# Kernel tuning notes

Hardware: AMD Instinct MI355X
Metric: run time of the kernel (lower is better)

The kernel has to match this reference:

```python
import jax, jax.numpy as jnp
import numpy as np

B, T, D, H = 64, 512, 256, 512  # batch, seq_len, embed_dim, enc_units


def _lstm(x_tbd, U, xW, reverse):
    """Keras LSTM with activation='sigmoid' (all gates AND candidate/output use sigmoid).
    x_tbd: [T,B,D] (only for shape), xW: precomputed x@W+b [T,B,4H], U: [H,4H].
    Gate order in Keras kernels: i, f, c(g), o."""
    if reverse:
        xW = xW[::-1]
    b = xW.shape[1]
    h0 = jnp.zeros((b, U.shape[0]), xW.dtype)
    c0 = jnp.zeros((b, U.shape[0]), xW.dtype)

    def step(carry, xw):
        h, c = carry
        z = xw + h @ U  # [B,4H]
        i, f, g, o = jnp.split(z, 4, axis=-1)
        i = jax.nn.sigmoid(i)
        f = jax.nn.sigmoid(f)
        g = jax.nn.sigmoid(g)  # activation='sigmoid' (not tanh)
        o = jax.nn.sigmoid(o)
        c_new = f * c + i * g
        h_new = o * jax.nn.sigmoid(c_new)  # activation='sigmoid' (not tanh)
        return (h_new, c_new), h_new

    (h_last, c_last), hs = jax.lax.scan(step, (h0, c0), xW)
    if reverse:
        hs = hs[::-1]  # Bidirectional re-reverses backward outputs to align in time
    return hs, h_last, c_last


def setup_inputs() -> dict:
    key = jax.random.key(0)
    ks = jax.random.split(key, 6)
    s_in = 1.0 / np.sqrt(D)
    s_rec = 1.0 / np.sqrt(H)
    return {
        "x": jax.random.normal(ks[0], (B, T, D), jnp.float32),
        "hidden": jax.random.normal(ks[1], (2 * B, H), jnp.float32),  # unused by call()
        "Wf": jax.random.normal(ks[2], (D, 4 * H), jnp.float32) * s_in,
        "Uf": jax.random.normal(ks[3], (H, 4 * H), jnp.float32) * s_rec,
        "bf": jnp.zeros((4 * H,), jnp.float32),
        "Wb": jax.random.normal(ks[4], (D, 4 * H), jnp.float32) * s_in,
        "Ub": jax.random.normal(ks[5], (H, 4 * H), jnp.float32) * s_rec,
        "bb": jnp.zeros((4 * H,), jnp.float32),
    }


def reference(x, hidden, Wf, Uf, bf, Wb, Ub, bb):
    x_tbd = jnp.transpose(x, (1, 0, 2))  # [T,B,D]
    # Precompute input projections for all timesteps (hoisted out of the scan)
    xWf = jnp.einsum('tbd,dh->tbh', x_tbd, Wf) + bf
    xWb = jnp.einsum('tbd,dh->tbh', x_tbd, Wb) + bb
    hs_f, hF, cF = _lstm(x_tbd, Uf, xWf, reverse=False)
    hs_b, hB, cB = _lstm(x_tbd, Ub, xWb, reverse=True)
    out = 0.5 * (hs_f + hs_b)  # merge_mode='ave'
    out = jnp.transpose(out, (1, 0, 2))  # [B,T,H]
    return out, hF, cF, hB, cB
```

## Files before the change

kernel.cpp:

```cpp
#include <hip/hip_runtime.h>
#include <hip/hip_bf16.h>
#include <cstdint>
#include <cstddef>

#define BB 64
#define TT 512
#define DD 256
#define HH 512
#define G4 2048

typedef __bf16 bf16x8 __attribute__((ext_vector_type(8)));
typedef __bf16 bf16x4 __attribute__((ext_vector_type(4)));
typedef float  f32x4  __attribute__((ext_vector_type(4)));
typedef unsigned long long ull_t;

#define TAGM 0xC000C000C000C000ULL

#define SPIN_CAP (1 << 16)

__device__ __forceinline__ float sigf(float x) {
  return 1.0f / (1.0f + __expf(-x));
}

__device__ __forceinline__ ull_t coh_load_u64(const __bf16* p) {
  return __hip_atomic_load(reinterpret_cast<const ull_t*>(p),
                           __ATOMIC_RELAXED, __HIP_MEMORY_SCOPE_AGENT);
}
__device__ __forceinline__ void coh_pub_u32(unsigned* p, unsigned v) {
  (void)__hip_atomic_exchange(p, v, __ATOMIC_RELAXED, __HIP_MEMORY_SCOPE_AGENT);
}

__global__ void cvt_x_kernel(const float* __restrict__ x, __bf16* __restrict__ xb) {
  int i = (blockIdx.x * 256 + threadIdx.x) * 4;
  float4 v = *(const float4*)(x + i);
  bf16x4 o;
  o[0] = (__bf16)v.x; o[1] = (__bf16)v.y; o[2] = (__bf16)v.z; o[3] = (__bf16)v.w;
  *(bf16x4*)(xb + i) = o;
}

__launch_bounds__(256, 1)
__global__ void lstm_kernel(const __bf16* __restrict__ xb,
                            const float* __restrict__ Wf, const float* __restrict__ Uf,
                            const float* __restrict__ bf_,
                            const float* __restrict__ Wb, const float* __restrict__ Ub,
                            const float* __restrict__ bb_,
                            __bf16* __restrict__ hbuf,
                            float* __restrict__ out,
                            __bf16* __restrict__ hsb) {
  const int bx  = blockIdx.x;
  const int dir = bx >> 5;
  const int s   = bx & 31;
  const float* Wd = dir ? Wb : Wf;
  const float* Ud = dir ? Ub : Uf;
  const float* bd = dir ? bb_ : bf_;
  __bf16* hb = hbuf + (size_t)dir * 2 * BB * HH;

  const int tid  = threadIdx.x;
  const int mt   = tid >> 6;
  const int lane = tid & 63;
  const int j    = lane & 15;
  const int q    = lane >> 4;
  const int colg = s * 16 + j;

  bf16x8 wfrag[4][24];
#pragma unroll
  for (int g = 0; g < 4; ++g) {
    const int col = g * HH + colg;
#pragma unroll
    for (int kt = 0; kt < 24; ++kt) {
      bf16x8 v;
#pragma unroll
      for (int e = 0; e < 8; ++e) {
        const int k = kt * 32 + q * 8 + e;
        const float w = (k < DD) ? Wd[(size_t)k * G4 + col]
                                 : Ud[(size_t)(k - DD) * G4 + col];
        v[e] = (__bf16)w;
      }
      wfrag[g][kt] = v;
    }
  }
  float bg[4];
#pragma unroll
  for (int g = 0; g < 4; ++g) bg[g] = bd[g * HH + colg];

  float cst[4] = {0.f, 0.f, 0.f, 0.f};
  const size_t outTail = (size_t)BB * TT * HH;

  for (int tau = 0; tau < TT; ++tau) {
    const int t = dir ? (TT - 1 - tau) : tau;

    const __bf16* xrow = xb + ((size_t)(mt * 16 + j) * TT + t) * DD + q * 8;
    f32x4 acc[4];
#pragma unroll
    for (int g = 0; g < 4; ++g) acc[g] = (f32x4){bg[g], bg[g], bg[g], bg[g]};
#pragma unroll
    for (int kt = 0; kt < 8; ++kt) {
      bf16x8 a = *(const bf16x8*)(xrow + kt * 32);
#pragma unroll
      for (int g = 0; g < 4; ++g)
        acc[g] = __builtin_amdgcn_mfma_f32_16x16x32_bf16(a, wfrag[g][kt], acc[g], 0, 0, 0);
    }

    if (tau) {
      const __bf16* hrow = hb + (size_t)(tau & 1) * (BB * HH)
                              + (size_t)(mt * 16 + j) * HH + q * 8;
      const ull_t epat = (ull_t)(1u + ((unsigned)(tau >> 1) & 1u)) * 0x4000400040004000ULL;
      ull_t cur[8], nxt[8];
#pragma unroll
      for (int i = 0; i < 4; ++i) {
        cur[2*i]   = coh_load_u64(hrow + i * 32);
        cur[2*i+1] = coh_load_u64(hrow + i * 32 + 4);
      }
#pragma unroll
      for (int kb = 0; kb < 4; ++kb) {
        if (kb < 3) {
#pragma unroll
          for (int i = 0; i < 4; ++i) {
            nxt[2*i]   = coh_load_u64(hrow + ((kb + 1) * 4 + i) * 32);
            nxt[2*i+1] = coh_load_u64(hrow + ((kb + 1) * 4 + i) * 32 + 4);
          }
        }
        int guard = 0;
        for (;;) {
          int ok = 1;
#pragma unroll
          for (int i = 0; i < 8; ++i) ok &= ((cur[i] & TAGM) == epat);
          if (__all(ok)) break;
          if (++guard > SPIN_CAP) break;
          __builtin_amdgcn_s_sleep(2);
#pragma unroll
          for (int i = 0; i < 4; ++i) {
            cur[2*i]   = coh_load_u64(hrow + (kb * 4 + i) * 32);
            cur[2*i+1] = coh_load_u64(hrow + (kb * 4 + i) * 32 + 4);
          }
        }
#pragma unroll
        for (int i = 0; i < 4; ++i) {
          union { ull_t u[2]; bf16x8 v; } uu;
          uu.u[0] = cur[2*i]   & ~TAGM;
          uu.u[1] = cur[2*i+1] & ~TAGM;
          const int kt = kb * 4 + i;
#pragma unroll
          for (int g = 0; g < 4; ++g)
            acc[g] = __builtin_amdgcn_mfma_f32_16x16x32_bf16(uu.v, wfrag[g][8 + kt], acc[g], 0, 0, 0);
        }
        if (kb < 3) {
#pragma unroll
          for (int i = 0; i < 8; ++i) cur[i] = nxt[i];
        }
      }
    }

    const unsigned ptag =
        ((1u + ((unsigned)((tau + 1) >> 1) & 1u)) << 14);
    __bf16* hnext = hb + (size_t)((tau + 1) & 1) * (BB * HH);
    unsigned myv[4];
#pragma unroll
    for (int r = 0; r < 4; ++r) {
      const float zi = acc[0][r], zf = acc[1][r], zg = acc[2][r], zo = acc[3][r];
      const float gi = sigf(zi), gf = sigf(zf), gg = sigf(zg), go = sigf(zo);
      const float cn = gf * cst[r] + gi * gg;
      cst[r] = cn;
      const float hn = go * sigf(cn);
      union { __bf16 b; unsigned short u; } cv;
      cv.b = (__bf16)hn;
      myv[r] = (unsigned)cv.u | ptag;
      const int orow = mt * 16 + q * 4 + r;
      if (dir == 0) {
        out[(size_t)orow * (TT * HH) + (size_t)t * HH + colg] = 0.5f * hn;
      } else {
        hsb[(size_t)t * (BB * HH) + (size_t)orow * HH + colg] = (__bf16)hn;
      }
      if (tau == TT - 1) {
        float* base = out + outTail + (size_t)dir * (2 * BB * HH);
        base[(size_t)orow * HH + colg] = hn;
        base[(size_t)BB * HH + (size_t)orow * HH + colg] = cn;
      }
    }

    unsigned pr[4];
#pragma unroll
    for (int r = 0; r < 4; ++r) pr[r] = __shfl_xor((int)myv[r], 1);
    if ((lane & 1) == 0) {
#pragma unroll
      for (int r = 0; r < 4; ++r) {
        const int orow = mt * 16 + q * 4 + r;
        unsigned pk = (myv[r] & 0xFFFFu) | (pr[r] << 16);
        coh_pub_u32((unsigned*)&hnext[(size_t)orow * HH + colg], pk);
      }
    }
  }
}

__global__ void combine_kernel(float* __restrict__ out, const __bf16* __restrict__ hsb) {
  const size_t i = ((size_t)blockIdx.x * 256 + threadIdx.x) * 4;
  const size_t b = i >> 18;
  const size_t t = (i >> 9) & 511;
  const size_t c = i & 511;
  bf16x4 hv = *(const bf16x4*)(hsb + t * (BB * HH) + b * HH + c);
  float4 v = *(float4*)(out + i);
  v.x += 0.5f * (float)hv[0];
  v.y += 0.5f * (float)hv[1];
  v.z += 0.5f * (float)hv[2];
  v.w += 0.5f * (float)hv[3];
  *(float4*)(out + i) = v;
}

extern "C" void kernel_launch(void* const* d_in, const int* in_sizes, int n_in,
                              void* d_out, int out_size, void* d_ws, size_t ws_size,
                              hipStream_t stream) {
  (void)in_sizes; (void)n_in; (void)out_size; (void)ws_size;
  const float* x   = (const float*)d_in[0];
  const float* Wf  = (const float*)d_in[2];
  const float* Uf  = (const float*)d_in[3];
  const float* bf_ = (const float*)d_in[4];
  const float* Wb  = (const float*)d_in[5];
  const float* Ub  = (const float*)d_in[6];
  const float* bb_ = (const float*)d_in[7];
  float* out = (float*)d_out;
  char* ws = (char*)d_ws;

  __bf16* hbuf = (__bf16*)(ws + 1024);
  __bf16* xb   = (__bf16*)(ws + (1 << 19));
  __bf16* hsb  = (__bf16*)(ws + (1 << 19) + (size_t)BB * TT * DD * 2);

  hipMemsetAsync(ws, 0xFF, 1 << 19, stream);
  cvt_x_kernel<<<dim3((BB * TT * DD) / 1024), dim3(256), 0, stream>>>(x, xb);
  lstm_kernel<<<dim3(64), dim3(256), 0, stream>>>(xb, Wf, Uf, bf_, Wb, Ub, bb_,
                                                  hbuf, out, hsb);
  combine_kernel<<<dim3((BB * TT * HH) / 1024), dim3(256), 0, stream>>>(out, hsb);
}
```

Before: 3.971 ms.

## Split LSTM recurrent K-reduction across two wave groups with LDS partial sums

Doubles the block to 512 threads and splits the K dimension of each timestep's gate matmul between two halves. One half computes the input projection plus the first 128 hidden columns, the other computes the remaining 384 hidden columns. Partial accumulators are reduced through shared memory after a __syncthreads. The goal is to halve the per-wave MFMA chain and register footprint on the serial critical path. The cost is an extra block-wide barrier and LDS traffic every step, with an uneven work split between the halves.

```diff
diff --git a/kernel.cpp b/kernel.cpp
--- a/kernel.cpp
+++ b/kernel.cpp
@@ -38,7 +38,7 @@
   *(bf16x4*)(xb + i) = o;
 }
 
-__launch_bounds__(256, 1)
+__launch_bounds__(512, 1)
 __global__ void lstm_kernel(const __bf16* __restrict__ xb,
                             const float* __restrict__ Wf, const float* __restrict__ Uf,
                             const float* __restrict__ bf_,
@@ -56,22 +56,26 @@
   __bf16* hb = hbuf + (size_t)dir * 2 * BB * HH;
 
   const int tid  = threadIdx.x;
-  const int mt   = tid >> 6;
+  const int mt   = (tid >> 6) & 3;
+  const int half = tid >> 8;
   const int lane = tid & 63;
   const int j    = lane & 15;
   const int q    = lane >> 4;
   const int colg = s * 16 + j;
 
-  bf16x8 wfrag[4][24];
+  __shared__ f32x4 partial[2][4][4][64];
+
+  bf16x8 wfrag[4][12];
 #pragma unroll
   for (int g = 0; g < 4; ++g) {
     const int col = g * HH + colg;
 #pragma unroll
-    for (int kt = 0; kt < 24; ++kt) {
+    for (int kt = 0; kt < 12; ++kt) {
+      const int ktg = half * 12 + kt;
       bf16x8 v;
 #pragma unroll
       for (int e = 0; e < 8; ++e) {
-        const int k = kt * 32 + q * 8 + e;
+        const int k = ktg * 32 + q * 8 + e;
         const float w = (k < DD) ? Wd[(size_t)k * G4 + col]
                                  : Ud[(size_t)(k - DD) * G4 + col];
         v[e] = (__bf16)w;
@@ -88,37 +92,28 @@
 
   for (int tau = 0; tau < TT; ++tau) {
     const int t = dir ? (TT - 1 - tau) : tau;
-
-    const __bf16* xrow = xb + ((size_t)(mt * 16 + j) * TT + t) * DD + q * 8;
+    const __bf16* hrow = hb + (size_t)(tau & 1) * (BB * HH)
+                            + (size_t)(mt * 16 + j) * HH + q * 8;
+    const ull_t epat = (ull_t)(1u + ((unsigned)(tau >> 1) & 1u)) * 0x4000400040004000ULL;
+
     f32x4 acc[4];
-#pragma unroll
-    for (int g = 0; g < 4; ++g) acc[g] = (f32x4){bg[g], bg[g], bg[g], bg[g]};
-#pragma unroll
-    for (int kt = 0; kt < 8; ++kt) {
-      bf16x8 a = *(const bf16x8*)(xrow + kt * 32);
-#pragma unroll
-      for (int g = 0; g < 4; ++g)
-        acc[g] = __builtin_amdgcn_mfma_f32_16x16x32_bf16(a, wfrag[g][kt], acc[g], 0, 0, 0);
-    }
-
-    if (tau) {
-      const __bf16* hrow = hb + (size_t)(tau & 1) * (BB * HH)
-                              + (size_t)(mt * 16 + j) * HH + q * 8;
-      const ull_t epat = (ull_t)(1u + ((unsigned)(tau >> 1) & 1u)) * 0x4000400040004000ULL;
-      ull_t cur[8], nxt[8];
-#pragma unroll
-      for (int i = 0; i < 4; ++i) {
-        cur[2*i]   = coh_load_u64(hrow + i * 32);
-        cur[2*i+1] = coh_load_u64(hrow + i * 32 + 4);
-      }
-#pragma unroll
-      for (int kb = 0; kb < 4; ++kb) {
-        if (kb < 3) {
-#pragma unroll
-          for (int i = 0; i < 4; ++i) {
-            nxt[2*i]   = coh_load_u64(hrow + ((kb + 1) * 4 + i) * 32);
-            nxt[2*i+1] = coh_load_u64(hrow + ((kb + 1) * 4 + i) * 32 + 4);
-          }
+    if (half == 0) {
+      const __bf16* xrow = xb + ((size_t)(mt * 16 + j) * TT + t) * DD + q * 8;
+#pragma unroll
+      for (int g = 0; g < 4; ++g) acc[g] = (f32x4){bg[g], bg[g], bg[g], bg[g]};
+#pragma unroll
+      for (int kt = 0; kt < 8; ++kt) {
+        bf16x8 a = *(const bf16x8*)(xrow + kt * 32);
+#pragma unroll
+        for (int g = 0; g < 4; ++g)
+          acc[g] = __builtin_amdgcn_mfma_f32_16x16x32_bf16(a, wfrag[g][kt], acc[g], 0, 0, 0);
+      }
+      if (tau) {
+        ull_t cur[8];
+#pragma unroll
+        for (int i = 0; i < 4; ++i) {
+          cur[2*i]   = coh_load_u64(hrow + i * 32);
+          cur[2*i+1] = coh_load_u64(hrow + i * 32 + 4);
         }
         int guard = 0;
         for (;;) {
@@ -130,8 +125,8 @@
           __builtin_amdgcn_s_sleep(2);
 #pragma unroll
           for (int i = 0; i < 4; ++i) {
-            cur[2*i]   = coh_load_u64(hrow + (kb * 4 + i) * 32);
-            cur[2*i+1] = coh_load_u64(hrow + (kb * 4 + i) * 32 + 4);
+            cur[2*i]   = coh_load_u64(hrow + i * 32);
+            cur[2*i+1] = coh_load_u64(hrow + i * 32 + 4);
           }
         }
 #pragma unroll
@@ -139,54 +134,107 @@
           union { ull_t u[2]; bf16x8 v; } uu;
           uu.u[0] = cur[2*i]   & ~TAGM;
           uu.u[1] = cur[2*i+1] & ~TAGM;
-          const int kt = kb * 4 + i;
 #pragma unroll
           for (int g = 0; g < 4; ++g)
-            acc[g] = __builtin_amdgcn_mfma_f32_16x16x32_bf16(uu.v, wfrag[g][8 + kt], acc[g], 0, 0, 0);
-        }
-        if (kb < 3) {
-#pragma unroll
-          for (int i = 0; i < 8; ++i) cur[i] = nxt[i];
-        }
-      }
+            acc[g] = __builtin_amdgcn_mfma_f32_16x16x32_bf16(uu.v, wfrag[g][8 + i], acc[g], 0, 0, 0);
+        }
+      }
+    } else {
+#pragma unroll
+      for (int g = 0; g < 4; ++g) acc[g] = (f32x4){0.f, 0.f, 0.f, 0.f};
+      if (tau) {
+        const __bf16* hrow1 = hrow + 128;
+        ull_t cur[8], nxt[8];
+#pragma unroll
+        for (int i = 0; i < 4; ++i) {
+          cur[2*i]   = coh_load_u64(hrow1 + i * 32);
+          cur[2*i+1] = coh_load_u64(hrow1 + i * 32 + 4);
+        }
+#pragma unroll
+        for (int kb = 0; kb < 3; ++kb) {
+          if (kb < 2) {
+#pragma unroll
+            for (int i = 0; i < 4; ++i) {
+              nxt[2*i]   = coh_load_u64(hrow1 + ((kb + 1) * 4 + i) * 32);
+              nxt[2*i+1] = coh_load_u64(hrow1 + ((kb + 1) * 4 + i) * 32 + 4);
+            }
+          }
+          int guard = 0;
+          for (;;) {
+            int ok = 1;
+#pragma unroll
+            for (int i = 0; i < 8; ++i) ok &= ((cur[i] & TAGM) == epat);
+            if (__all(ok)) break;
+            if (++guard > SPIN_CAP) break;
+            __builtin_amdgcn_s_sleep(2);
+#pragma unroll
+            for (int i = 0; i < 4; ++i) {
+              cur[2*i]   = coh_load_u64(hrow1 + (kb * 4 + i) * 32);
+              cur[2*i+1] = coh_load_u64(hrow1 + (kb * 4 + i) * 32 + 4);
+            }
+          }
+#pragma unroll
+          for (int i = 0; i < 4; ++i) {
+            union { ull_t u[2]; bf16x8 v; } uu;
+            uu.u[0] = cur[2*i]   & ~TAGM;
+            uu.u[1] = cur[2*i+1] & ~TAGM;
+#pragma unroll
+            for (int g = 0; g < 4; ++g)
+              acc[g] = __builtin_amdgcn_mfma_f32_16x16x32_bf16(uu.v, wfrag[g][kb * 4 + i], acc[g], 0, 0, 0);
+          }
+          if (kb < 2) {
+#pragma unroll
+            for (int i = 0; i < 8; ++i) cur[i] = nxt[i];
+          }
+        }
+      }
+#pragma unroll
+      for (int g = 0; g < 4; ++g) partial[tau & 1][mt][g][lane] = acc[g];
     }
 
-    const unsigned ptag =
-        ((1u + ((unsigned)((tau + 1) >> 1) & 1u)) << 14);
-    __bf16* hnext = hb + (size_t)((tau + 1) & 1) * (BB * HH);
-    unsigned myv[4];
-#pragma unroll
-    for (int r = 0; r < 4; ++r) {
-      const float zi = acc[0][r], zf = acc[1][r], zg = acc[2][r], zo = acc[3][r];
-      const float gi = sigf(zi), gf = sigf(zf), gg = sigf(zg), go = sigf(zo);
-      const float cn = gf * cst[r] + gi * gg;
-      cst[r] = cn;
-      const float hn = go * sigf(cn);
-      union { __bf16 b; unsigned short u; } cv;
-      cv.b = (__bf16)hn;
-      myv[r] = (unsigned)cv.u | ptag;
-      const int orow = mt * 16 + q * 4 + r;
-      if (dir == 0) {
-        out[(size_t)orow * (TT * HH) + (size_t)t * HH + colg] = 0.5f * hn;
-      } else {
-        hsb[(size_t)t * (BB * HH) + (size_t)orow * HH + colg] = (__bf16)hn;
-      }
-      if (tau == TT - 1) {
-        float* base = out + outTail + (size_t)dir * (2 * BB * HH);
-        base[(size_t)orow * HH + colg] = hn;
-        base[(size_t)BB * HH + (size_t)orow * HH + colg] = cn;
-      }
-    }
-
-    unsigned pr[4];
-#pragma unroll
-    for (int r = 0; r < 4; ++r) pr[r] = __shfl_xor((int)myv[r], 1);
-    if ((lane & 1) == 0) {
+    __syncthreads();
+
+    if (half == 0) {
+#pragma unroll
+      for (int g = 0; g < 4; ++g) {
+        f32x4 p = partial[tau & 1][mt][g][lane];
+        acc[g] += p;
+      }
+      const unsigned ptag = ((1u + ((unsigned)((tau + 1) >> 1) & 1u)) << 14);
+      __bf16* hnext = hb + (size_t)((tau + 1) & 1) * (BB * HH);
+      unsigned myv[4];
 #pragma unroll
       for (int r = 0; r < 4; ++r) {
+        const float zi = acc[0][r], zf = acc[1][r], zg = acc[2][r], zo = acc[3][r];
+        const float gi = sigf(zi), gf = sigf(zf), gg = sigf(zg), go = sigf(zo);
+        const float cn = gf * cst[r] + gi * gg;
+        cst[r] = cn;
+        const float hn = go * sigf(cn);
+        union { __bf16 b; unsigned short u; } cv;
+        cv.b = (__bf16)hn;
+        myv[r] = (unsigned)cv.u | ptag;
         const int orow = mt * 16 + q * 4 + r;
-        unsigned pk = (myv[r] & 0xFFFFu) | (pr[r] << 16);
-        coh_pub_u32((unsigned*)&hnext[(size_t)orow * HH + colg], pk);
+        if (dir == 0) {
+          out[(size_t)orow * (TT * HH) + (size_t)t * HH + colg] = 0.5f * hn;
+        } else {
+          hsb[(size_t)t * (BB * HH) + (size_t)orow * HH + colg] = (__bf16)hn;
+        }
+        if (tau == TT - 1) {
+          float* base = out + outTail + (size_t)dir * (2 * BB * HH);
+          base[(size_t)orow * HH + colg] = hn;
+          base[(size_t)BB * HH + (size_t)orow * HH + colg] = cn;
+        }
+      }
+      unsigned pr[4];
+#pragma unroll
+      for (int r = 0; r < 4; ++r) pr[r] = __shfl_xor((int)myv[r], 1);
+      if ((lane & 1) == 0) {
+#pragma unroll
+        for (int r = 0; r < 4; ++r) {
+          const int orow = mt * 16 + q * 4 + r;
+          unsigned pk = (myv[r] & 0xFFFFu) | (pr[r] << 16);
+          coh_pub_u32((unsigned*)&hnext[(size_t)orow * HH + colg], pk);
+        }
       }
     }
   }
@@ -226,7 +274,7 @@
 
   hipMemsetAsync(ws, 0xFF, 1 << 19, stream);
   cvt_x_kernel<<<dim3((BB * TT * DD) / 1024), dim3(256), 0, stream>>>(x, xb);
-  lstm_kernel<<<dim3(64), dim3(256), 0, stream>>>(xb, Wf, Uf, bf_, Wb, Ub, bb_,
+  lstm_kernel<<<dim3(64), dim3(512), 0, stream>>>(xb, Wf, Uf, bf_, Wb, Ub, bb_,
                                                   hbuf, out, hsb);
   combine_kernel<<<dim3((BB * TT * HH) / 1024), dim3(256), 0, stream>>>(out, hsb);
 }
```

Result: slower. 7.026 ms (+76.9%).

## Split LSTM across 256 blocks with 4 hidden columns each and shuffle gate exchange

Applied to the files above, without the earlier changes.

Changes the persistent LSTM from 64 to 256 workgroups (128 per direction). Each block now owns 4 hidden columns, with all four gates packed into one 16-wide MFMA tile, where it previously owned 16 columns. Gates are exchanged between lanes with xor shuffles, which cuts per-wave MFMA work and weight registers by four. All h loads for a step are issued up front before the x projection so their latency is hidden, and the spin sleep is shortened. In exchange, four times as many blocks must synchronise through the global flag protocol every step, and only a quarter of the lanes store outputs.

```diff
diff --git a/kernel.cpp b/kernel.cpp
--- a/kernel.cpp
+++ b/kernel.cpp
@@ -48,8 +48,8 @@
                             float* __restrict__ out,
                             __bf16* __restrict__ hsb) {
   const int bx  = blockIdx.x;
-  const int dir = bx >> 5;
-  const int s   = bx & 31;
+  const int dir = bx >> 7;
+  const int s   = bx & 127;
   const float* Wd = dir ? Wb : Wf;
   const float* Ud = dir ? Ub : Uf;
   const float* bd = dir ? bb_ : bf_;
@@ -60,128 +60,128 @@
   const int lane = tid & 63;
   const int j    = lane & 15;
   const int q    = lane >> 4;
-  const int colg = s * 16 + j;
-
-  bf16x8 wfrag[4][24];
-#pragma unroll
-  for (int g = 0; g < 4; ++g) {
-    const int col = g * HH + colg;
-#pragma unroll
-    for (int kt = 0; kt < 24; ++kt) {
-      bf16x8 v;
-#pragma unroll
-      for (int e = 0; e < 8; ++e) {
-        const int k = kt * 32 + q * 8 + e;
-        const float w = (k < DD) ? Wd[(size_t)k * G4 + col]
-                                 : Ud[(size_t)(k - DD) * G4 + col];
-        v[e] = (__bf16)w;
-      }
-      wfrag[g][kt] = v;
-    }
+  const int gt   = j >> 2;
+  const int u    = j & 3;
+  const int colg = s * 4 + u;
+
+  bf16x8 wfrag[24];
+#pragma unroll
+  for (int kt = 0; kt < 24; ++kt) {
+    const int col = gt * HH + colg;
+    bf16x8 v;
+#pragma unroll
+    for (int e = 0; e < 8; ++e) {
+      const int k = kt * 32 + q * 8 + e;
+      const float w = (k < DD) ? Wd[(size_t)k * G4 + col]
+                               : Ud[(size_t)(k - DD) * G4 + col];
+      v[e] = (__bf16)w;
+    }
+    wfrag[kt] = v;
   }
-  float bg[4];
-#pragma unroll
-  for (int g = 0; g < 4; ++g) bg[g] = bd[g * HH + colg];
+  const float bg = bd[gt * HH + colg];
 
   float cst[4] = {0.f, 0.f, 0.f, 0.f};
   const size_t outTail = (size_t)BB * TT * HH;
 
   for (int tau = 0; tau < TT; ++tau) {
     const int t = dir ? (TT - 1 - tau) : tau;
+    const __bf16* hrow = hb + (size_t)(tau & 1) * (BB * HH)
+                            + (size_t)(mt * 16 + j) * HH + q * 8;
+    const ull_t epat = (ull_t)(1u + ((unsigned)(tau >> 1) & 1u)) * 0x4000400040004000ULL;
+
+    ull_t hld[32];
+    if (tau) {
+#pragma unroll
+      for (int kt = 0; kt < 16; ++kt) {
+        hld[2*kt]   = coh_load_u64(hrow + kt * 32);
+        hld[2*kt+1] = coh_load_u64(hrow + kt * 32 + 4);
+      }
+    }
 
     const __bf16* xrow = xb + ((size_t)(mt * 16 + j) * TT + t) * DD + q * 8;
-    f32x4 acc[4];
-#pragma unroll
-    for (int g = 0; g < 4; ++g) acc[g] = (f32x4){bg[g], bg[g], bg[g], bg[g]};
+    f32x4 acc = (f32x4){bg, bg, bg, bg};
 #pragma unroll
     for (int kt = 0; kt < 8; ++kt) {
       bf16x8 a = *(const bf16x8*)(xrow + kt * 32);
-#pragma unroll
-      for (int g = 0; g < 4; ++g)
-        acc[g] = __builtin_amdgcn_mfma_f32_16x16x32_bf16(a, wfrag[g][kt], acc[g], 0, 0, 0);
+      acc = __builtin_amdgcn_mfma_f32_16x16x32_bf16(a, wfrag[kt], acc, 0, 0, 0);
     }
 
     if (tau) {
-      const __bf16* hrow = hb + (size_t)(tau & 1) * (BB * HH)
-                              + (size_t)(mt * 16 + j) * HH + q * 8;
-      const ull_t epat = (ull_t)(1u + ((unsigned)(tau >> 1) & 1u)) * 0x4000400040004000ULL;
-      ull_t cur[8], nxt[8];
-#pragma unroll
-      for (int i = 0; i < 4; ++i) {
-        cur[2*i]   = coh_load_u64(hrow + i * 32);
-        cur[2*i+1] = coh_load_u64(hrow + i * 32 + 4);
-      }
 #pragma unroll
       for (int kb = 0; kb < 4; ++kb) {
-        if (kb < 3) {
-#pragma unroll
-          for (int i = 0; i < 4; ++i) {
-            nxt[2*i]   = coh_load_u64(hrow + ((kb + 1) * 4 + i) * 32);
-            nxt[2*i+1] = coh_load_u64(hrow + ((kb + 1) * 4 + i) * 32 + 4);
-          }
-        }
         int guard = 0;
         for (;;) {
           int ok = 1;
 #pragma unroll
-          for (int i = 0; i < 8; ++i) ok &= ((cur[i] & TAGM) == epat);
+          for (int i = 0; i < 8; ++i) ok &= ((hld[kb * 8 + i] & TAGM) == epat);
           if (__all(ok)) break;
           if (++guard > SPIN_CAP) break;
-          __builtin_amdgcn_s_sleep(2);
+          __builtin_amdgcn_s_sleep(1);
 #pragma unroll
           for (int i = 0; i < 4; ++i) {
-            cur[2*i]   = coh_load_u64(hrow + (kb * 4 + i) * 32);
-            cur[2*i+1] = coh_load_u64(hrow + (kb * 4 + i) * 32 + 4);
+            hld[kb*8 + 2*i]   = coh_load_u64(hrow + (kb * 4 + i) * 32);
+            hld[kb*8 + 2*i+1] = coh_load_u64(hrow + (kb * 4 + i) * 32 + 4);
           }
         }
 #pragma unroll
         for (int i = 0; i < 4; ++i) {
-          union { ull_t u[2]; bf16x8 v; } uu;
-          uu.u[0] = cur[2*i]   & ~TAGM;
-          uu.u[1] = cur[2*i+1] & ~TAGM;
-          const int kt = kb * 4 + i;
-#pragma unroll
-          for (int g = 0; g < 4; ++g)
-            acc[g] = __builtin_amdgcn_mfma_f32_16x16x32_bf16(uu.v, wfrag[g][8 + kt], acc[g], 0, 0, 0);
-        }
-        if (kb < 3) {
-#pragma unroll
-          for (int i = 0; i < 8; ++i) cur[i] = nxt[i];
-        }
-      }
-    }
-
-    const unsigned ptag =
-        ((1u + ((unsigned)((tau + 1) >> 1) & 1u)) << 14);
+          union { ull_t uq[2]; bf16x8 v; } uu;
+          uu.uq[0] = hld[kb*8 + 2*i]   & ~TAGM;
+          uu.uq[1] = hld[kb*8 + 2*i+1] & ~TAGM;
+          acc = __builtin_amdgcn_mfma_f32_16x16x32_bf16(uu.v, wfrag[8 + kb * 4 + i], acc, 0, 0, 0);
+        }
+      }
+    }
+
+    f32x4 vb, vc, vd;
+#pragma unroll
+    for (int e = 0; e < 4; ++e) {
+      vb[e] = __shfl_xor(acc[e], 4);
+      vc[e] = __shfl_xor(acc[e], 8);
+      vd[e] = __shfl_xor(vb[e], 8);
+    }
+    const bool p  = (gt & 1) != 0;
+    const bool h2 = (gt & 2) != 0;
+
+    const unsigned ptag = ((1u + ((unsigned)((tau + 1) >> 1) & 1u)) << 14);
     __bf16* hnext = hb + (size_t)((tau + 1) & 1) * (BB * HH);
     unsigned myv[4];
 #pragma unroll
     for (int r = 0; r < 4; ++r) {
-      const float zi = acc[0][r], zf = acc[1][r], zg = acc[2][r], zo = acc[3][r];
+      const float i1 = p ? vb[r] : acc[r];
+      const float i2 = p ? vd[r] : vc[r];
+      const float iA = p ? acc[r] : vb[r];
+      const float iB = p ? vc[r] : vd[r];
+      const float zi = h2 ? i2 : i1;
+      const float zf = h2 ? iB : iA;
+      const float zg = h2 ? i1 : i2;
+      const float zo = h2 ? iA : iB;
       const float gi = sigf(zi), gf = sigf(zf), gg = sigf(zg), go = sigf(zo);
       const float cn = gf * cst[r] + gi * gg;
       cst[r] = cn;
       const float hn = go * sigf(cn);
-      union { __bf16 b; unsigned short u; } cv;
+      union { __bf16 b; unsigned short us; } cv;
       cv.b = (__bf16)hn;
-      myv[r] = (unsigned)cv.u | ptag;
-      const int orow = mt * 16 + q * 4 + r;
-      if (dir == 0) {
-        out[(size_t)orow * (TT * HH) + (size_t)t * HH + colg] = 0.5f * hn;
-      } else {
-        hsb[(size_t)t * (BB * HH) + (size_t)orow * HH + colg] = (__bf16)hn;
-      }
-      if (tau == TT - 1) {
-        float* base = out + outTail + (size_t)dir * (2 * BB * HH);
-        base[(size_t)orow * HH + colg] = hn;
-        base[(size_t)BB * HH + (size_t)orow * HH + colg] = cn;
+      myv[r] = (unsigned)cv.us | ptag;
+      if (gt == 0) {
+        const int orow = mt * 16 + q * 4 + r;
+        if (dir == 0) {
+          out[(size_t)orow * (TT * HH) + (size_t)t * HH + colg] = 0.5f * hn;
+        } else {
+          hsb[(size_t)t * (BB * HH) + (size_t)orow * HH + colg] = (__bf16)hn;
+        }
+        if (tau == TT - 1) {
+          float* base = out + outTail + (size_t)dir * (2 * BB * HH);
+          base[(size_t)orow * HH + colg] = hn;
+          base[(size_t)BB * HH + (size_t)orow * HH + colg] = cn;
+        }
       }
     }
 
     unsigned pr[4];
 #pragma unroll
     for (int r = 0; r < 4; ++r) pr[r] = __shfl_xor((int)myv[r], 1);
-    if ((lane & 1) == 0) {
+    if (gt == 0 && (u & 1) == 0) {
 #pragma unroll
       for (int r = 0; r < 4; ++r) {
         const int orow = mt * 16 + q * 4 + r;
@@ -226,7 +226,7 @@
 
   hipMemsetAsync(ws, 0xFF, 1 << 19, stream);
   cvt_x_kernel<<<dim3((BB * TT * DD) / 1024), dim3(256), 0, stream>>>(x, xb);
-  lstm_kernel<<<dim3(64), dim3(256), 0, stream>>>(xb, Wf, Uf, bf_, Wb, Ub, bb_,
-                                                  hbuf, out, hsb);
+  lstm_kernel<<<dim3(256), dim3(256), 0, stream>>>(xb, Wf, Uf, bf_, Wb, Ub, bb_,
+                                                   hbuf, out, hsb);
   combine_kernel<<<dim3((BB * TT * HH) / 1024), dim3(256), 0, stream>>>(out, hsb);
 }
```

Result: slower. 11.74 ms (+195.5%).
